# Performance work log

Measured on AMD Instinct MI355X. Metric: run time of the kernel, lower is better.

The kernel has to match this reference:

```python
import jax, jax.numpy as jnp
import numpy as np

N, NUM_TOKENS, TOKEN_DIM = 32768, 8192, 768
K = 4  # hard-coded top-k in the torch forward


def setup_inputs() -> dict:
    key = jax.random.key(0)
    k1, k2 = jax.random.split(key)
    inputs_flatten = jax.random.normal(k1, (N, TOKEN_DIM), dtype=jnp.float32)
    embed = jax.random.normal(k2, (NUM_TOKENS, TOKEN_DIM), dtype=jnp.float32)  # codebook buffer
    return {"inputs_flatten": inputs_flatten, "embed": embed}


def reference(inputs_flatten, embed):
    # squared euclidean distances: [N, num_tokens]
    distances = (
        jnp.sum(inputs_flatten ** 2, axis=1, keepdims=True)
        + jnp.sum(embed ** 2, axis=1)
        - 2.0 * (inputs_flatten @ embed.T)
    )

    # k smallest distances via top_k on negated distances
    neg_vals, topk_indices = jax.lax.top_k(-distances, K)
    topk_values = -neg_vals  # ascending smallest-k distances, [N, 4]

    # drop nearest, reweight the next 3 neighbors
    tv = topk_values[:, 1:]  # [N, 3]
    tv = tv / jnp.maximum(jnp.linalg.norm(tv, axis=1, keepdims=True), 1e-12)  # F.normalize
    tv = 1.0 / (tv + 1e-4)
    topk_values = jax.nn.softmax(tv, axis=1)
    topk_indices_out = topk_indices[:, 1:]

    # hard assignment (argmin) and codebook lookup (one-hot scatter + matmul == gather)
    encoding_indices = jnp.argmin(distances, axis=1)[:, None]  # [N, 1]
    quantize = embed[encoding_indices[:, 0]]  # [N, token_dim]

    # straight-through estimator
    quantize = jax.lax.stop_gradient(quantize - inputs_flatten) + inputs_flatten
    return quantize, encoding_indices, topk_values, topk_indices_out
```

## Files before the change

kernel.cpp:

```cpp
#include <hip/hip_runtime.h>
#include <cfloat>
#include <cmath>

#define NROWS 32768
#define NTOK  8192
#define DIM   768
#define KSPLIT 384

#define BM 64
#define BN 128
#define BK 32
#define NT 512

#define Q_OFF   0
#define EI_OFF  (NROWS*DIM)
#define TV_OFF  (EI_OFF + NROWS)
#define TI_OFF  (TV_OFF + NROWS*3)

typedef short short8 __attribute__((ext_vector_type(8)));
typedef float f32x4 __attribute__((ext_vector_type(4)));
typedef float f32x16 __attribute__((ext_vector_type(16)));

__global__ __launch_bounds__(256)
void np_norm_kernel(const float* __restrict__ x, float* __restrict__ o) {
#pragma clang fp contract(off)
  const int wid = (blockIdx.x * 256 + threadIdx.x) >> 6;
  const int lane = threadIdx.x & 63;
  const float* p = x + (size_t)wid * DIM + (lane >> 3) * 96 + (lane & 7);
  float v = p[0];
  float r = v * v;
#pragma unroll
  for (int k = 1; k < 12; k++) {
    float w = p[8 * k];
    float sq = w * w;
    r = r + sq;
  }
#pragma unroll
  for (int m = 1; m < 64; m <<= 1) {
    float other = __shfl_xor(r, m, 64);
    r = r + other;
  }
  if (lane == 0) o[wid] = r;
}

__device__ __forceinline__ bool dless(float a, int ai, float b, int bi_) {
  return (a < b) || (a == b && ai < bi_);
}

__device__ __forceinline__ void ins4(float (&v)[4], int (&x)[4], float c, int ci) {
  if (dless(c, ci, v[3], x[3])) {
    v[3] = c; x[3] = ci;
    if (dless(v[3], x[3], v[2], x[2])) { float tv = v[2]; int ti = x[2]; v[2] = v[3]; x[2] = x[3]; v[3] = tv; x[3] = ti; }
    if (dless(v[2], x[2], v[1], x[1])) { float tv = v[1]; int ti = x[1]; v[1] = v[2]; x[1] = x[2]; v[2] = tv; x[2] = ti; }
    if (dless(v[1], x[1], v[0], x[0])) { float tv = v[0]; int ti = x[0]; v[0] = v[1]; x[0] = x[1]; v[1] = tv; x[1] = ti; }
  }
}

__device__ __forceinline__ void ins8(float (&v)[8], int (&x)[8], float c, int ci) {
  if (dless(c, ci, v[7], x[7])) {
    v[7] = c; x[7] = ci;
#pragma unroll
    for (int k = 7; k > 0; k--) {
      if (dless(v[k], x[k], v[k - 1], x[k - 1])) {
        float tv = v[k - 1]; int ti = x[k - 1];
        v[k - 1] = v[k]; x[k - 1] = x[k];
        v[k] = tv; x[k] = ti;
      }
    }
  }
}

__device__ __forceinline__ unsigned short f2bf(float f) {
  unsigned int u = __float_as_uint(f);
  u += 0x7FFFu + ((u >> 16) & 1u);
  return (unsigned short)(u >> 16);
}

typedef const __attribute__((address_space(1))) void* gas1_t;
typedef __attribute__((address_space(3))) void* las3_t;
__device__ __forceinline__ void gl16(const void* g, void* s) {
  __builtin_amdgcn_global_load_lds((gas1_t)g, (las3_t)s, 16, 0, 0);
}

__global__ __launch_bounds__(256)
void cvtT_kernel(const float* __restrict__ in, unsigned short* __restrict__ out, int nrows) {
  const int row = blockIdx.x * 256 + threadIdx.x;
  const int Q = blockIdx.y;
  const float4* p = (const float4*)(in + (size_t)row * DIM + Q * 8);
  const float4 a = p[0], b = p[1];
  union { unsigned short u[8]; int4 v; } pk;
  pk.u[0] = f2bf(a.x); pk.u[1] = f2bf(a.y); pk.u[2] = f2bf(a.z); pk.u[3] = f2bf(a.w);
  pk.u[4] = f2bf(b.x); pk.u[5] = f2bf(b.y); pk.u[6] = f2bf(b.z); pk.u[7] = f2bf(b.w);
  *(int4*)(out + ((size_t)Q * nrows + row) * 8) = pk.v;
}

#define STRIPS 16
#define KSTEPS 24
#define NITER (STRIPS * KSTEPS)

__global__ __launch_bounds__(512, 2)
void vq_rank(const unsigned short* __restrict__ xbT, const unsigned short* __restrict__ ebT,
             const float* __restrict__ e2g, unsigned short* __restrict__ topp) {
  __shared__ __align__(16) unsigned char xsm[4][16384];
  __shared__ __align__(16) unsigned char esm[4][16384];
  __shared__ __align__(16) float e2s[4096];

  const int tid = threadIdx.x;
  const int l = tid & 63;
  const int w = tid >> 6;
  const int wr = w >> 1, wc = w & 1;
  const int l31 = l & 31, h = l >> 5;

  const int bid = (int)blockIdx.x;
  const int sbid = (bid & 7) * 32 + (bid >> 3);
  const int rb = sbid >> 1;
  const int chalf = sbid & 1;
  const int row0 = rb * 256;
  const int cg0 = chalf * 4096;

  const int st_kq = w >> 2;
  const int st_idx = (w & 3) * 64 + l;
  const size_t xbase = (size_t)st_kq * NROWS * 8 + ((size_t)(row0 + st_idx)) * 8;
  const size_t ebase = (size_t)st_kq * NTOK * 8 + ((size_t)(cg0 + st_idx)) * 8;

  float bv[2][8]; int bi[2][8];
#pragma unroll
  for (int xj = 0; xj < 2; ++xj)
#pragma unroll
    for (int c = 0; c < 8; ++c) { bv[xj][c] = FLT_MAX; bi[xj][c] = 0x7FFFFFFF; }

  f32x16 acc[4][2];
#pragma unroll
  for (int ei = 0; ei < 4; ++ei)
#pragma unroll
    for (int xj = 0; xj < 2; ++xj) acc[ei][xj] = (f32x16)0.f;

#define STAGE(buf, SKK, SCOFF)                                                  \
  {                                                                             \
    const unsigned short* xs = xbT + xbase + ((size_t)(SKK) << 20);             \
    gl16(xs, &xsm[buf][(w * 64) * 16]);                                         \
    gl16(xs + NROWS * 16, &xsm[buf][(512 + w * 64) * 16]);                      \
    const unsigned short* es = ebT + ebase + ((size_t)(SKK) << 18) +            \
                               ((size_t)(SCOFF) << 3);                          \
    gl16(es, &esm[buf][(w * 64) * 16]);                                         \
    gl16(es + NTOK * 16, &esm[buf][(512 + w * 64) * 16]);                       \
  }

#define COMPUTE(b)                                                              \
  {                                                                             \
    const unsigned char* xb = &xsm[b][0];                                       \
    const unsigned char* ebp = &esm[b][0];                                      \
    _Pragma("unroll")                                                           \
    for (int s = 0; s < 2; ++s) {                                               \
      const int kqo = (s * 2 + h) * 256;                                        \
      short8 af[4], bfr[2];                                                     \
      _Pragma("unroll")                                                         \
      for (int ei = 0; ei < 4; ++ei)                                            \
        af[ei] = *(const short8*)(ebp + (size_t)(kqo + wc * 128 + ei * 32 + l31) * 16); \
      _Pragma("unroll")                                                         \
      for (int xj = 0; xj < 2; ++xj)                                            \
        bfr[xj] = *(const short8*)(xb + (size_t)(kqo + wr * 64 + xj * 32 + l31) * 16); \
      _Pragma("unroll")                                                         \
      for (int ei = 0; ei < 4; ++ei)                                            \
        _Pragma("unroll")                                                       \
        for (int xj = 0; xj < 2; ++xj)                                          \
          acc[ei][xj] = __builtin_amdgcn_mfma_f32_32x32x16_bf16(af[ei], bfr[xj], acc[ei][xj], 0, 0, 0); \
    }                                                                           \
  }

#define SELECT                                                                  \
  {                                                                             \
    _Pragma("unroll")                                                           \
    for (int ei = 0; ei < 4; ++ei) {                                            \
      float4 e2q[4];                                                            \
      _Pragma("unroll")                                                         \
      for (int q = 0; q < 4; ++q)                                               \
        e2q[q] = *(const float4*)&e2s[selb + wc * 128 + ei * 32 + q * 8 + 4 * h]; \
      const int cb = cg0 + selb + wc * 128 + ei * 32 + 4 * h;                   \
      _Pragma("unroll")                                                         \
      for (int xj = 0; xj < 2; ++xj) {                                          \
        float sv[16];                                                           \
        _Pragma("unroll")                                                       \
        for (int q = 0; q < 4; ++q) {                                           \
          sv[q * 4 + 0] = fmaf(-2.f, acc[ei][xj][q * 4 + 0], e2q[q].x);         \
          sv[q * 4 + 1] = fmaf(-2.f, acc[ei][xj][q * 4 + 1], e2q[q].y);         \
          sv[q * 4 + 2] = fmaf(-2.f, acc[ei][xj][q * 4 + 2], e2q[q].z);         \
          sv[q * 4 + 3] = fmaf(-2.f, acc[ei][xj][q * 4 + 3], e2q[q].w);         \
        }                                                                       \
        float mn = sv[0];                                                       \
        _Pragma("unroll")                                                       \
        for (int r = 1; r < 16; ++r) mn = fminf(mn, sv[r]);                     \
        if (mn < bv[xj][7]) {                                                   \
          _Pragma("unroll")                                                     \
          for (int q = 0; q < 4; ++q)                                           \
            _Pragma("unroll")                                                   \
            for (int j = 0; j < 4; ++j)                                         \
              ins8(bv[xj], bi[xj], sv[q * 4 + j], cb + q * 8 + j);              \
        }                                                                       \
      }                                                                         \
    }                                                                           \
    _Pragma("unroll")                                                           \
    for (int ei = 0; ei < 4; ++ei)                                              \
      _Pragma("unroll")                                                         \
      for (int xj = 0; xj < 2; ++xj) acc[ei][xj] = (f32x16)0.f;                 \
  }

#define WAIT8 { asm volatile("s_waitcnt vmcnt(8)" ::: "memory"); __builtin_amdgcn_s_barrier(); asm volatile("" ::: "memory"); }
#define WAIT4 { asm volatile("s_waitcnt vmcnt(4)" ::: "memory"); __builtin_amdgcn_s_barrier(); asm volatile("" ::: "memory"); }
#define WAIT0 { asm volatile("s_waitcnt vmcnt(0)" ::: "memory"); __builtin_amdgcn_s_barrier(); asm volatile("" ::: "memory"); }

#pragma unroll
  for (int c = 0; c < 2; ++c) {
    const int f = c * 512 + w * 64;
    gl16((const unsigned char*)e2g + (size_t)cg0 * 4 + (size_t)(f + l) * 16,
         (unsigned char*)e2s + f * 16);
  }
  STAGE(0, 0, 0)
  STAGE(1, 1, 0)
  STAGE(2, 2, 0)
  WAIT8

  int skk = 3, scoff = 0;
  int kc = 0, selb = 0;

#define BODY_MAIN(b)                                                            \
  {                                                                             \
    STAGE(((b) + 3) & 3, skk, scoff)                                            \
    if (++skk == KSTEPS) { skk = 0; scoff += 256; }                             \
    COMPUTE(b)                                                                  \
    if (++kc == KSTEPS) { SELECT kc = 0; selb += 256; }                         \
    WAIT8                                                                       \
  }

  for (int t = 0; t < NITER - 12; t += 4) {
    BODY_MAIN(0)
    BODY_MAIN(1)
    BODY_MAIN(2)
    BODY_MAIN(3)
  }

#pragma unroll
  for (int tt = 0; tt < 12; ++tt) {
    const int t = NITER - 12 + tt;
    const int b = t & 3;
    if (t + 3 < NITER) {
      STAGE((b + 3) & 3, skk, scoff)
      if (++skk == KSTEPS) { skk = 0; scoff += 256; }
    }
    COMPUTE(b)
    if (++kc == KSTEPS) { SELECT kc = 0; selb += 256; }
    if (t + 3 < NITER) { WAIT8 }
    else if (t + 2 < NITER) { WAIT4 }
    else if (t + 1 < NITER) { WAIT0 }
  }
#undef BODY_MAIN
#undef WAIT8
#undef WAIT4
#undef WAIT0
#undef SELECT
#undef COMPUTE
#undef STAGE

#pragma unroll
  for (int xj = 0; xj < 2; ++xj) {
    float ov[8]; int oi[8];
#pragma unroll
    for (int c = 0; c < 8; ++c) {
      ov[c] = __shfl_xor(bv[xj][c], 32, 64);
      oi[c] = __shfl_xor(bi[xj][c], 32, 64);
    }
#pragma unroll
    for (int c = 0; c < 8; ++c) ins8(bv[xj], bi[xj], ov[c], oi[c]);
  }

  __syncthreads();
  float* mval = (float*)&xsm[0][0];
  int* midx = (int*)&esm[0][0];
  if (l < 32) {
#pragma unroll
    for (int xj = 0; xj < 2; ++xj) {
      const int rr = wr * 64 + xj * 32 + l31;
#pragma unroll
      for (int c = 0; c < 8; ++c) {
        mval[(wc * 256 + rr) * 8 + c] = bv[xj][c];
        midx[(wc * 256 + rr) * 8 + c] = bi[xj][c];
      }
    }
  }
  __syncthreads();
  if (wc == 0 && l < 32) {
#pragma unroll
    for (int xj = 0; xj < 2; ++xj) {
      const int rr = wr * 64 + xj * 32 + l31;
      const float* ov = &mval[(256 + rr) * 8];
      const int* oi = &midx[(256 + rr) * 8];
#pragma unroll
      for (int c = 0; c < 8; ++c) ins8(bv[xj], bi[xj], ov[c], oi[c]);
      unsigned short* dst = topp + (size_t)(row0 + rr) * 16 + chalf * 8;
#pragma unroll
      for (int c = 0; c < 8; ++c) dst[c] = (unsigned short)bi[xj][c];
    }
  }
}

__global__ __launch_bounds__(256)
void vq_refine16(const float* __restrict__ x, const float* __restrict__ E,
                 const float* __restrict__ x2, const float* __restrict__ e2,
                 const unsigned short* __restrict__ topp, float* __restrict__ out) {
  const int gid = blockIdx.x * 256 + threadIdx.x;
  const int row = gid >> 4;
  const int s = gid & 15;
  const int myc = topp[(size_t)row * 16 + s];

  const float4* xr = (const float4*)(x + (size_t)row * DIM);
  const float4* er = (const float4*)(E + (size_t)myc * DIM);
  float accA = 0.f, accB = 0.f;
#pragma unroll 8
  for (int q = 0; q < KSPLIT / 4; ++q) {
    const float4 a = xr[q], b = er[q];
    accA = fmaf(a.x, b.x, accA); accA = fmaf(a.y, b.y, accA);
    accA = fmaf(a.z, b.z, accA); accA = fmaf(a.w, b.w, accA);
  }
#pragma unroll 8
  for (int q = KSPLIT / 4; q < DIM / 4; ++q) {
    const float4 a = xr[q], b = er[q];
    accB = fmaf(a.x, b.x, accB); accB = fmaf(a.y, b.y, accB);
    accB = fmaf(a.z, b.z, accB); accB = fmaf(a.w, b.w, accB);
  }
  const float d = fmaf(-2.0f, accA + accB, x2[row] + e2[myc]);

  const int base = (threadIdx.x & 63) & ~15;
  float dv[16]; int cv[16];
#pragma unroll
  for (int t = 0; t < 16; ++t) {
    dv[t] = __shfl(d, base + t, 64);
    cv[t] = __shfl(myc, base + t, 64);
  }
#pragma unroll
  for (int a = 0; a < 4; ++a)
#pragma unroll
    for (int b = 15; b > a; --b) {
      const bool sw = (dv[b] < dv[b - 1]) || (dv[b] == dv[b - 1] && cv[b] < cv[b - 1]);
      if (sw) {
        float td = dv[b]; dv[b] = dv[b - 1]; dv[b - 1] = td;
        int ti = cv[b]; cv[b] = cv[b - 1]; cv[b - 1] = ti;
      }
    }

  if (s == 0) {
    out[EI_OFF + row] = (float)cv[0];
    const double d1 = (double)dv[1], d2 = (double)dv[2], d3 = (double)dv[3];
    double nrm = sqrt(d1 * d1 + d2 * d2 + d3 * d3);
    nrm = fmax(nrm, 1e-12);
    const double t1 = 1.0 / (d1 / nrm + 1e-4);
    const double t2 = 1.0 / (d2 / nrm + 1e-4);
    const double t3 = 1.0 / (d3 / nrm + 1e-4);
    const double mx = fmax(t1, fmax(t2, t3));
    const double e1 = exp(t1 - mx), e2x = exp(t2 - mx), e3 = exp(t3 - mx);
    const double sm = e1 + e2x + e3;
    out[TV_OFF + row * 3 + 0] = (float)(e1 / sm);
    out[TV_OFF + row * 3 + 1] = (float)(e2x / sm);
    out[TV_OFF + row * 3 + 2] = (float)(e3 / sm);
    out[TI_OFF + row * 3 + 0] = (float)cv[1];
    out[TI_OFF + row * 3 + 1] = (float)cv[2];
    out[TI_OFF + row * 3 + 2] = (float)cv[3];
  }

  const float4* src = (const float4*)(E + (size_t)cv[0] * DIM);
  float4* dst = (float4*)(out + Q_OFF + (size_t)row * DIM);
#pragma unroll
  for (int k = 0; k < 12; ++k) dst[s + k * 16] = src[s + k * 16];
}

__global__ __launch_bounds__(NT, 4)
void vq_main(const float* __restrict__ A, const float* __restrict__ E,
             const float* __restrict__ x2, const float* __restrict__ e2,
             float* __restrict__ out) {
  __shared__ float a_s[BK][BM + 4];
  __shared__ float b_s[BK][BN + 4];

  const int tid = threadIdx.x;
  const int tx = tid & 15;
  const int ty = tid >> 4;
  const int row0 = blockIdx.x * BM;

  const float x2r[2] = { x2[row0 + ty * 2 + 0], x2[row0 + ty * 2 + 1] };

  float bv[2][4];
  int   bi[2][4];
#pragma unroll
  for (int i = 0; i < 2; i++)
#pragma unroll
    for (int c = 0; c < 4; c++) { bv[i][c] = FLT_MAX; bi[i][c] = 0x7FFFFFFF; }

#define GEMM_STEP(k0, ACC)                                                       \
    {                                                                            \
      __syncthreads();                                                           \
      {                                                                          \
        const int r = tid >> 3, kq = tid & 7;                                    \
        const float4 v = *(const float4*)(A + (size_t)(row0 + r) * DIM + (k0 + kq * 4)); \
        a_s[kq * 4 + 0][r] = v.x; a_s[kq * 4 + 1][r] = v.y;                      \
        a_s[kq * 4 + 2][r] = v.z; a_s[kq * 4 + 3][r] = v.w;                      \
        _Pragma("unroll")                                                        \
        for (int s = 0; s < 2; s++) {                                            \
          const int fi = tid + s * NT;                                           \
          const int rb = fi >> 3, kb = fi & 7;                                   \
          const float4 w = *(const float4*)(E + (size_t)(col0 + rb) * DIM + (k0 + kb * 4)); \
          b_s[kb * 4 + 0][rb] = w.x; b_s[kb * 4 + 1][rb] = w.y;                  \
          b_s[kb * 4 + 2][rb] = w.z; b_s[kb * 4 + 3][rb] = w.w;                  \
        }                                                                        \
      }                                                                          \
      __syncthreads();                                                           \
      _Pragma("unroll")                                                          \
      for (int k = 0; k < BK; k++) {                                             \
        const float2 a2 = *(const float2*)&a_s[k][ty * 2];                       \
        float br[8];                                                             \
        *(float4*)(br)     = *(const float4*)&b_s[k][tx * 8];                    \
        *(float4*)(br + 4) = *(const float4*)&b_s[k][tx * 8 + 4];                \
        _Pragma("unroll")                                                        \
        for (int j = 0; j < 8; j++) {                                            \
          ACC[0][j] = fmaf(a2.x, br[j], ACC[0][j]);                              \
          ACC[1][j] = fmaf(a2.y, br[j], ACC[1][j]);                              \
        }                                                                        \
      }                                                                          \
    }

  for (int ct = 0; ct < NTOK / BN; ++ct) {
    const int col0 = ct * BN;

    float accA[2][8], accB[2][8];
#pragma unroll
    for (int i = 0; i < 2; i++)
#pragma unroll
      for (int j = 0; j < 8; j++) { accA[i][j] = 0.f; accB[i][j] = 0.f; }

    for (int k0 = 0; k0 < KSPLIT; k0 += BK) GEMM_STEP(k0, accA)
    for (int k0 = KSPLIT; k0 < DIM; k0 += BK) GEMM_STEP(k0, accB)

    float e2v[8];
    *(float4*)(e2v)     = *(const float4*)(e2 + col0 + tx * 8);
    *(float4*)(e2v + 4) = *(const float4*)(e2 + col0 + tx * 8 + 4);
#pragma unroll
    for (int i = 0; i < 2; i++) {
#pragma unroll
      for (int j = 0; j < 8; j++) {
        const float dot = accA[i][j] + accB[i][j];
        const float se = x2r[i] + e2v[j];
        const float d = fmaf(-2.0f, dot, se);
        const int ci = col0 + tx * 8 + j;
        ins4(bv[i], bi[i], d, ci);
      }
    }
  }
#undef GEMM_STEP

#pragma unroll
  for (int m = 1; m < 16; m <<= 1) {
#pragma unroll
    for (int i = 0; i < 2; i++) {
      float ov[4]; int oi[4];
#pragma unroll
      for (int c = 0; c < 4; c++) {
        ov[c] = __shfl_xor(bv[i][c], m, 64);
        oi[c] = __shfl_xor(bi[i][c], m, 64);
      }
#pragma unroll
      for (int c = 0; c < 4; c++) ins4(bv[i], bi[i], ov[c], oi[c]);
    }
  }

#pragma unroll
  for (int i = 0; i < 2; i++) {
    if (tx == i) {
      const int gr = row0 + ty * 2 + i;
      out[EI_OFF + gr] = (float)bi[i][0];
      const double d1 = (double)bv[i][1], d2 = (double)bv[i][2], d3 = (double)bv[i][3];
      double nrm = sqrt(d1 * d1 + d2 * d2 + d3 * d3);
      nrm = fmax(nrm, 1e-12);
      const double t1 = 1.0 / (d1 / nrm + 1e-4);
      const double t2 = 1.0 / (d2 / nrm + 1e-4);
      const double t3 = 1.0 / (d3 / nrm + 1e-4);
      const double mx = fmax(t1, fmax(t2, t3));
      const double e1 = exp(t1 - mx), e2x = exp(t2 - mx), e3 = exp(t3 - mx);
      const double s = e1 + e2x + e3;
      out[TV_OFF + gr * 3 + 0] = (float)(e1 / s);
      out[TV_OFF + gr * 3 + 1] = (float)(e2x / s);
      out[TV_OFF + gr * 3 + 2] = (float)(e3 / s);
      out[TI_OFF + gr * 3 + 0] = (float)bi[i][1];
      out[TI_OFF + gr * 3 + 1] = (float)bi[i][2];
      out[TI_OFF + gr * 3 + 2] = (float)bi[i][3];
    }
  }

  __syncthreads();
  int* idx_sh = (int*)&a_s[0][0];
  if (tx == 0) idx_sh[ty * 2 + 0] = bi[0][0];
  if (tx == 1) idx_sh[ty * 2 + 1] = bi[1][0];
  __syncthreads();

  for (int f = tid; f < BM * (DIM / 4); f += NT) {
    const int r = f / (DIM / 4);
    const int c = f % (DIM / 4);
    const int e = idx_sh[r];
    const float4 v = *(const float4*)(E + (size_t)e * DIM + c * 4);
    *(float4*)(out + Q_OFF + (size_t)(row0 + r) * DIM + c * 4) = v;
  }
}

extern "C" void kernel_launch(void* const* d_in, const int* in_sizes, int n_in,
                              void* d_out, int out_size, void* d_ws, size_t ws_size,
                              hipStream_t stream) {
  const float* x = (const float*)d_in[0];
  const float* E = (const float*)d_in[1];
  float* out = (float*)d_out;

  unsigned char* ws = (unsigned char*)d_ws;
  float* e2 = (float*)ws;
  float* x2 = (float*)(ws + 32768);
  unsigned short* topp = (unsigned short*)(ws + 32768 + 131072);
  unsigned short* xbT = (unsigned short*)(ws + 32768 + 131072 + 1048576);
  unsigned short* ebT = xbT + (size_t)NROWS * DIM;
  const size_t need = 32768 + 131072 + 1048576 +
                      (size_t)NROWS * DIM * 2 + (size_t)NTOK * DIM * 2;

  np_norm_kernel<<<NTOK / 4, 256, 0, stream>>>(E, e2);
  np_norm_kernel<<<NROWS / 4, 256, 0, stream>>>(x, x2);

  if (ws_size >= need) {
    cvtT_kernel<<<dim3(NROWS / 256, DIM / 8), 256, 0, stream>>>(x, xbT, NROWS);
    cvtT_kernel<<<dim3(NTOK / 256, DIM / 8), 256, 0, stream>>>(E, ebT, NTOK);
    vq_rank<<<256, 512, 0, stream>>>(xbT, ebT, e2, topp);
    vq_refine16<<<NROWS * 16 / 256, 256, 0, stream>>>(x, E, x2, e2, topp, out);
  } else {
    vq_main<<<NROWS / BM, NT, 0, stream>>>(x, E, x2, e2, out);
  }
}
```

Before: 1.101 ms.

## Restructure vq_rank into 256-thread blocks with 128-row tiles and double buffering

The ranking GEMM kernel changes from 512-thread blocks covering 256 rows to 256-thread blocks covering 128 rows, launched as 512 blocks. Its four-stage LDS pipeline with partial vmcnt waits becomes a simpler two-buffer loop that waits fully for loads each iteration. The LDS copy of e2 is dropped, so SELECT reads e2 directly from global memory, and s_setprio is raised around the MFMA section. The goal is smaller LDS use and more blocks for better occupancy and scheduling. The cost is less load/compute overlap, a full vmcnt(0) stall per step, and global loads for e2.

```diff
diff --git a/kernel.cpp b/kernel.cpp
--- a/kernel.cpp
+++ b/kernel.cpp
@@ -98,12 +98,11 @@
 #define KSTEPS 24
 #define NITER (STRIPS * KSTEPS)
 
-__global__ __launch_bounds__(512, 2)
+__global__ __launch_bounds__(256, 2)
 void vq_rank(const unsigned short* __restrict__ xbT, const unsigned short* __restrict__ ebT,
              const float* __restrict__ e2g, unsigned short* __restrict__ topp) {
-  __shared__ __align__(16) unsigned char xsm[4][16384];
-  __shared__ __align__(16) unsigned char esm[4][16384];
-  __shared__ __align__(16) float e2s[4096];
+  __shared__ __align__(16) unsigned char esm[2][16384];
+  __shared__ __align__(16) unsigned char xsm[2][8192];
 
   const int tid = threadIdx.x;
   const int l = tid & 63;
@@ -112,16 +111,12 @@
   const int l31 = l & 31, h = l >> 5;
 
   const int bid = (int)blockIdx.x;
-  const int sbid = (bid & 7) * 32 + (bid >> 3);
-  const int rb = sbid >> 1;
-  const int chalf = sbid & 1;
-  const int row0 = rb * 256;
+  const int sbid = (bid & 7) * 64 + (bid >> 3);
+  const int chalf = sbid >> 8;
+  const int row0 = (sbid & 255) * 128;
   const int cg0 = chalf * 4096;
 
-  const int st_kq = w >> 2;
-  const int st_idx = (w & 3) * 64 + l;
-  const size_t xbase = (size_t)st_kq * NROWS * 8 + ((size_t)(row0 + st_idx)) * 8;
-  const size_t ebase = (size_t)st_kq * NTOK * 8 + ((size_t)(cg0 + st_idx)) * 8;
+  const int t7 = tid >> 7, t127 = tid & 127;
 
   float bv[2][8]; int bi[2][8];
 #pragma unroll
@@ -135,48 +130,51 @@
 #pragma unroll
     for (int xj = 0; xj < 2; ++xj) acc[ei][xj] = (f32x16)0.f;
 
-#define STAGE(buf, SKK, SCOFF)                                                  \
+#define STAGE(BN_, KT, COL0)                                                    \
   {                                                                             \
-    const unsigned short* xs = xbT + xbase + ((size_t)(SKK) << 20);             \
-    gl16(xs, &xsm[buf][(w * 64) * 16]);                                         \
-    gl16(xs + NROWS * 16, &xsm[buf][(512 + w * 64) * 16]);                      \
-    const unsigned short* es = ebT + ebase + ((size_t)(SKK) << 18) +            \
-                               ((size_t)(SCOFF) << 3);                          \
-    gl16(es, &esm[buf][(w * 64) * 16]);                                         \
-    gl16(es + NTOK * 16, &esm[buf][(512 + w * 64) * 16]);                       \
-  }
-
-#define COMPUTE(b)                                                              \
+    const unsigned short* eg = ebT + ((size_t)(4 * (KT)) * NTOK + (COL0) + tid) * 8; \
+    gl16(eg,                 &esm[BN_][(0 * 256 + w * 64) * 16]);               \
+    gl16(eg + NTOK * 8,      &esm[BN_][(1 * 256 + w * 64) * 16]);               \
+    gl16(eg + 2 * NTOK * 8,  &esm[BN_][(2 * 256 + w * 64) * 16]);               \
+    gl16(eg + 3 * NTOK * 8,  &esm[BN_][(3 * 256 + w * 64) * 16]);               \
+    const unsigned short* xg = xbT + ((size_t)(4 * (KT) + t7) * NROWS + row0 + t127) * 8; \
+    gl16(xg,                 &xsm[BN_][(0 * 256 + w * 64) * 16]);               \
+    gl16(xg + 2 * NROWS * 8, &xsm[BN_][(1 * 256 + w * 64) * 16]);               \
+  }
+
+#define COMPUTE(B_)                                                             \
   {                                                                             \
-    const unsigned char* xb = &xsm[b][0];                                       \
-    const unsigned char* ebp = &esm[b][0];                                      \
+    const unsigned char* ebp = &esm[B_][0];                                     \
+    const unsigned char* xbp = &xsm[B_][0];                                     \
+    __builtin_amdgcn_s_setprio(1);                                              \
     _Pragma("unroll")                                                           \
     for (int s = 0; s < 2; ++s) {                                               \
-      const int kqo = (s * 2 + h) * 256;                                        \
+      const int kq = s * 2 + h;                                                 \
       short8 af[4], bfr[2];                                                     \
       _Pragma("unroll")                                                         \
       for (int ei = 0; ei < 4; ++ei)                                            \
-        af[ei] = *(const short8*)(ebp + (size_t)(kqo + wc * 128 + ei * 32 + l31) * 16); \
+        af[ei] = *(const short8*)(ebp + (size_t)(kq * 256 + wc * 128 + ei * 32 + l31) * 16); \
       _Pragma("unroll")                                                         \
       for (int xj = 0; xj < 2; ++xj)                                            \
-        bfr[xj] = *(const short8*)(xb + (size_t)(kqo + wr * 64 + xj * 32 + l31) * 16); \
+        bfr[xj] = *(const short8*)(xbp + (size_t)(kq * 128 + wr * 64 + xj * 32 + l31) * 16); \
       _Pragma("unroll")                                                         \
       for (int ei = 0; ei < 4; ++ei)                                            \
         _Pragma("unroll")                                                       \
         for (int xj = 0; xj < 2; ++xj)                                          \
           acc[ei][xj] = __builtin_amdgcn_mfma_f32_32x32x16_bf16(af[ei], bfr[xj], acc[ei][xj], 0, 0, 0); \
     }                                                                           \
-  }
-
-#define SELECT                                                                  \
+    __builtin_amdgcn_s_setprio(0);                                              \
+  }
+
+#define SELECT(SC0)                                                             \
   {                                                                             \
     _Pragma("unroll")                                                           \
     for (int ei = 0; ei < 4; ++ei) {                                            \
+      const int cb = (SC0) + wc * 128 + ei * 32 + 4 * h;                        \
       float4 e2q[4];                                                            \
       _Pragma("unroll")                                                         \
       for (int q = 0; q < 4; ++q)                                               \
-        e2q[q] = *(const float4*)&e2s[selb + wc * 128 + ei * 32 + q * 8 + 4 * h]; \
-      const int cb = cg0 + selb + wc * 128 + ei * 32 + 4 * h;                   \
+        e2q[q] = *(const float4*)(e2g + cb + q * 8);                            \
       _Pragma("unroll")                                                         \
       for (int xj = 0; xj < 2; ++xj) {                                          \
         float sv[16];                                                           \
@@ -205,58 +203,28 @@
       for (int xj = 0; xj < 2; ++xj) acc[ei][xj] = (f32x16)0.f;                 \
   }
 
-#define WAIT8 { asm volatile("s_waitcnt vmcnt(8)" ::: "memory"); __builtin_amdgcn_s_barrier(); asm volatile("" ::: "memory"); }
-#define WAIT4 { asm volatile("s_waitcnt vmcnt(4)" ::: "memory"); __builtin_amdgcn_s_barrier(); asm volatile("" ::: "memory"); }
-#define WAIT0 { asm volatile("s_waitcnt vmcnt(0)" ::: "memory"); __builtin_amdgcn_s_barrier(); asm volatile("" ::: "memory"); }
-
-#pragma unroll
-  for (int c = 0; c < 2; ++c) {
-    const int f = c * 512 + w * 64;
-    gl16((const unsigned char*)e2g + (size_t)cg0 * 4 + (size_t)(f + l) * 16,
-         (unsigned char*)e2s + f * 16);
-  }
-  STAGE(0, 0, 0)
-  STAGE(1, 1, 0)
-  STAGE(2, 2, 0)
-  WAIT8
-
-  int skk = 3, scoff = 0;
-  int kc = 0, selb = 0;
-
-#define BODY_MAIN(b)                                                            \
-  {                                                                             \
-    STAGE(((b) + 3) & 3, skk, scoff)                                            \
-    if (++skk == KSTEPS) { skk = 0; scoff += 256; }                             \
-    COMPUTE(b)                                                                  \
-    if (++kc == KSTEPS) { SELECT kc = 0; selb += 256; }                         \
-    WAIT8                                                                       \
-  }
-
-  for (int t = 0; t < NITER - 12; t += 4) {
-    BODY_MAIN(0)
-    BODY_MAIN(1)
-    BODY_MAIN(2)
-    BODY_MAIN(3)
-  }
-
-#pragma unroll
-  for (int tt = 0; tt < 12; ++tt) {
-    const int t = NITER - 12 + tt;
-    const int b = t & 3;
-    if (t + 3 < NITER) {
-      STAGE((b + 3) & 3, skk, scoff)
-      if (++skk == KSTEPS) { skk = 0; scoff += 256; }
-    }
-    COMPUTE(b)
-    if (++kc == KSTEPS) { SELECT kc = 0; selb += 256; }
-    if (t + 3 < NITER) { WAIT8 }
-    else if (t + 2 < NITER) { WAIT4 }
-    else if (t + 1 < NITER) { WAIT0 }
-  }
-#undef BODY_MAIN
-#undef WAIT8
-#undef WAIT4
-#undef WAIT0
+  STAGE(0, 0, cg0)
+  asm volatile("s_waitcnt vmcnt(0)" ::: "memory");
+  __builtin_amdgcn_s_barrier();
+  asm volatile("" ::: "memory");
+
+  int cur = 0;
+  int nkt = 1, ncol0 = cg0;
+  int kc = 0, scol0 = cg0;
+
+#pragma unroll 1
+  for (int t = 0; t < NITER; ++t) {
+    if (t + 1 < NITER) {
+      STAGE(cur ^ 1, nkt, ncol0)
+      if (++nkt == KSTEPS) { nkt = 0; ncol0 += 256; }
+    }
+    COMPUTE(cur)
+    if (++kc == KSTEPS) { SELECT(scol0) kc = 0; scol0 += 256; }
+    asm volatile("s_waitcnt vmcnt(0)" ::: "memory");
+    __builtin_amdgcn_s_barrier();
+    asm volatile("" ::: "memory");
+    cur ^= 1;
+  }
 #undef SELECT
 #undef COMPUTE
 #undef STAGE
@@ -274,16 +242,16 @@
   }
 
   __syncthreads();
-  float* mval = (float*)&xsm[0][0];
-  int* midx = (int*)&esm[0][0];
-  if (l < 32) {
+  float* mval = (float*)&esm[0][0];
+  int*   midx = (int*)&xsm[0][0];
+  if (wc == 1 && l < 32) {
 #pragma unroll
     for (int xj = 0; xj < 2; ++xj) {
       const int rr = wr * 64 + xj * 32 + l31;
 #pragma unroll
       for (int c = 0; c < 8; ++c) {
-        mval[(wc * 256 + rr) * 8 + c] = bv[xj][c];
-        midx[(wc * 256 + rr) * 8 + c] = bi[xj][c];
+        mval[rr * 8 + c] = bv[xj][c];
+        midx[rr * 8 + c] = bi[xj][c];
       }
     }
   }
@@ -292,10 +260,8 @@
 #pragma unroll
     for (int xj = 0; xj < 2; ++xj) {
       const int rr = wr * 64 + xj * 32 + l31;
-      const float* ov = &mval[(256 + rr) * 8];
-      const int* oi = &midx[(256 + rr) * 8];
-#pragma unroll
-      for (int c = 0; c < 8; ++c) ins8(bv[xj], bi[xj], ov[c], oi[c]);
+#pragma unroll
+      for (int c = 0; c < 8; ++c) ins8(bv[xj], bi[xj], mval[rr * 8 + c], midx[rr * 8 + c]);
       unsigned short* dst = topp + (size_t)(row0 + rr) * 16 + chalf * 8;
 #pragma unroll
       for (int c = 0; c < 8; ++c) dst[c] = (unsigned short)bi[xj][c];
@@ -529,7 +495,7 @@
   if (ws_size >= need) {
     cvtT_kernel<<<dim3(NROWS / 256, DIM / 8), 256, 0, stream>>>(x, xbT, NROWS);
     cvtT_kernel<<<dim3(NTOK / 256, DIM / 8), 256, 0, stream>>>(E, ebT, NTOK);
-    vq_rank<<<256, 512, 0, stream>>>(xbT, ebT, e2, topp);
+    vq_rank<<<512, 256, 0, stream>>>(xbT, ebT, e2, topp);
     vq_refine16<<<NROWS * 16 / 256, 256, 0, stream>>>(x, E, x2, e2, topp, out);
   } else {
     vq_main<<<NROWS / BM, NT, 0, stream>>>(x, E, x2, e2, out);
```

Measured after the change: 1.141 ms. 3.6% more time.
